# Optimization experiments

Measured on AMD Instinct MI355X. Metric: run time of the kernel, lower is better.

The kernel has to match this reference:

```python
import jax, jax.numpy as jnp
import numpy as np

B, T, D, H = 2, 2048, 1024, 16
DH = D // H


def setup_inputs() -> dict:
    key = jax.random.key(0)
    ks = jax.random.split(key, 5)
    s = 1.0 / np.sqrt(D)
    return {
        "x": jax.random.normal(ks[0], (B, T, D), dtype=jnp.float32),
        "Wq": jax.random.normal(ks[1], (D, D), dtype=jnp.float32) * s,
        "Wk": jax.random.normal(ks[2], (D, D), dtype=jnp.float32) * s,
        "Wv": jax.random.normal(ks[3], (D, D), dtype=jnp.float32) * s,
        "Wo": jax.random.normal(ks[4], (D, D), dtype=jnp.float32) * s,
    }


def reference(x, Wq, Wk, Wv, Wo):
    # torch nn.Linear(bias=False): y = x @ W.T, weight shape [out, in]
    q = (x @ Wq.T).reshape(B, T, H, DH).transpose(0, 2, 1, 3)  # [B,H,T,Dh]
    k = (x @ Wk.T).reshape(B, T, H, DH).transpose(0, 2, 1, 3)
    v = (x @ Wv.T).reshape(B, T, H, DH).transpose(0, 2, 1, 3)
    scores = jnp.einsum("bhqd,bhkd->bhqk", q, k) / jnp.sqrt(jnp.float32(DH))
    att = jax.nn.softmax(scores, axis=-1)
    y = jnp.einsum("bhqk,bhkd->bhqd", att, v)  # [B,H,T,Dh]
    y = y.transpose(0, 2, 1, 3).reshape(B, T, D)
    return y @ Wo.T
```

## Files before the change

kernel.cpp:

```cpp
#include <hip/hip_runtime.h>
#include <math.h>

typedef __attribute__((ext_vector_type(8))) _Float16 half8;
typedef __attribute__((ext_vector_type(4))) _Float16 half4;
typedef __attribute__((ext_vector_type(4))) float f32x4;

namespace {
constexpr int T_ = 2048, DH_ = 64;
constexpr int M_ = 4096;
constexpr int KD = 1024;
}

__global__ __launch_bounds__(256)
void conv_half4(const float* __restrict__ s0, const float* __restrict__ s1,
                const float* __restrict__ s2, const float* __restrict__ s3,
                _Float16* __restrict__ dst)
{
    const float* s = (blockIdx.y == 0) ? s0 : (blockIdx.y == 1) ? s1
                   : (blockIdx.y == 2) ? s2 : s3;
    const size_t i = ((size_t)blockIdx.x * 256 + threadIdx.x) * 8;
    const float4 a = *reinterpret_cast<const float4*>(s + i);
    const float4 b = *reinterpret_cast<const float4*>(s + i + 4);
    half8 h;
    h[0] = (_Float16)a.x; h[1] = (_Float16)a.y; h[2] = (_Float16)a.z; h[3] = (_Float16)a.w;
    h[4] = (_Float16)b.x; h[5] = (_Float16)b.y; h[6] = (_Float16)b.z; h[7] = (_Float16)b.w;
    *reinterpret_cast<half8*>(dst + (size_t)blockIdx.y * 1048576 + i) = h;
}

template <int BN>
__global__ __launch_bounds__(256)
void gemm_half(const _Float16* __restrict__ A, const _Float16* __restrict__ Bw,
               float* __restrict__ Cout,
               _Float16* __restrict__ qh, _Float16* __restrict__ kh,
               _Float16* __restrict__ vh, const int mode)
{
    constexpr int NF = BN / 32;
    __shared__ _Float16 As[128 * 64];
    __shared__ _Float16 Bs[BN * 64];
    const int tid = threadIdx.x;
    const int l   = tid & 63;
    const int w   = tid >> 6;
    const int wm  = w >> 1, wn = w & 1;
    const int m0  = blockIdx.y * 128;
    const int n0  = blockIdx.x * BN;

    f32x4 acc[4][NF];
#pragma unroll
    for (int i = 0; i < 4; ++i)
#pragma unroll
        for (int j = 0; j < NF; ++j) acc[i][j] = (f32x4){0.f, 0.f, 0.f, 0.f};

    const int srow = l >> 3;
    const int scol = ((l & 7) ^ srow) << 3;
    const int frow = l & 15;
    const int fkb  = (l >> 4) << 4;

    for (int kt = 0; kt < 16; ++kt) {
        const int kOff = kt << 6;
#pragma unroll
        for (int s = 0; s < 4; ++s) {
            const int j = (w << 2) + s;
            const _Float16* gp = A + (size_t)(m0 + (j << 3) + srow) * KD + kOff + scol;
            __builtin_amdgcn_global_load_lds(
                (const __attribute__((address_space(1))) void*)gp,
                (__attribute__((address_space(3))) void*)(As + (j << 9)), 16, 0, 0);
        }
#pragma unroll
        for (int s = 0; s < BN / 32; ++s) {
            const int j = w * (BN / 32) + s;
            const _Float16* gp = Bw + (size_t)(n0 + (j << 3) + srow) * KD + kOff + scol;
            __builtin_amdgcn_global_load_lds(
                (const __attribute__((address_space(1))) void*)gp,
                (__attribute__((address_space(3))) void*)(Bs + (j << 9)), 16, 0, 0);
        }
        __syncthreads();
#pragma unroll
        for (int ks = 0; ks < 2; ++ks) {
            half8 af[4], bfr[NF];
#pragma unroll
            for (int fi = 0; fi < 4; ++fi) {
                const int row = wm * 64 + fi * 16 + frow;
                const int cb  = (ks * 64 + fkb) ^ ((row & 7) << 4);
                af[fi] = *reinterpret_cast<const half8*>(
                    reinterpret_cast<const char*>(As) + row * 128 + cb);
            }
#pragma unroll
            for (int fj = 0; fj < NF; ++fj) {
                const int row = wn * (NF * 16) + fj * 16 + frow;
                const int cb  = (ks * 64 + fkb) ^ ((row & 7) << 4);
                bfr[fj] = *reinterpret_cast<const half8*>(
                    reinterpret_cast<const char*>(Bs) + row * 128 + cb);
            }
#pragma unroll
            for (int fi = 0; fi < 4; ++fi)
#pragma unroll
                for (int fj = 0; fj < NF; ++fj)
                    acc[fi][fj] = __builtin_amdgcn_mfma_f32_16x16x32_f16(
                        af[fi], bfr[fj], acc[fi][fj], 0, 0, 0);
        }
        __syncthreads();
    }

    const int r0 = (l >> 4) << 2;
    const float QSC = 0.125f * 1.44269504f;
#pragma unroll
    for (int fi = 0; fi < 4; ++fi)
#pragma unroll
        for (int fj = 0; fj < NF; ++fj)
#pragma unroll
            for (int r = 0; r < 4; ++r) {
                const int m = m0 + wm * 64 + fi * 16 + r0 + r;
                const int n = n0 + wn * (NF * 16) + fj * 16 + (l & 15);
                const float vv = acc[fi][fj][r];
                if (mode == 0) {
                    const int bb = m >> 11, t = m & 2047;
                    const int which = n >> 10, nl = n & 1023;
                    const int hh = nl >> 6, dh = nl & 63;
                    const int bh = (bb << 4) + hh;
                    if (which == 0)
                        qh[(((size_t)bh << 11) + t) * 64 + dh] = (_Float16)(vv * QSC);
                    else if (which == 1)
                        kh[(((size_t)bh << 11) + t) * 64 + dh] = (_Float16)vv;
                    else
                        vh[(((size_t)bh << 6) + dh) * 2048 + t] = (_Float16)vv;
                } else {
                    Cout[(size_t)m * 1024 + n] = vv;
                }
            }
}

#define SWZ(row, bytecol) (((row) << 7) + ((bytecol) ^ (((row) & 7) << 4)))

__global__ __launch_bounds__(256)
void attn_mfma(const _Float16* __restrict__ Qh, const _Float16* __restrict__ Kh,
               const _Float16* __restrict__ Vh, _Float16* __restrict__ Yh)
{
    __shared__ _Float16 Ks[2][64 * 64];
    __shared__ _Float16 Vs[2][64 * 64];
    __shared__ _Float16 Ps[64 * 64];
    const int tid = threadIdx.x;
    const int l   = tid & 63;
    const int w   = tid >> 6;
    const int g4  = l >> 4;
    const int c16 = l & 15;
    const int bh  = blockIdx.y;
    const int t0  = blockIdx.x * 64;
    const size_t qkbase = (size_t)bh * T_ * DH_;
    const size_t vbase  = (size_t)bh * DH_ * T_;

    const int srow = l >> 3;
    const int scol = ((l & 7) ^ srow) << 3;

    half8 qf[2];
#pragma unroll
    for (int ks = 0; ks < 2; ++ks)
        qf[ks] = *reinterpret_cast<const half8*>(
            Qh + qkbase + (size_t)(t0 + w * 16 + c16) * 64 + ks * 32 + g4 * 8);

    half8 ones;
#pragma unroll
    for (int j = 0; j < 8; ++j) ones[j] = (_Float16)1.f;

#pragma unroll
    for (int s = 0; s < 2; ++s) {
        const int j   = (w << 1) + s;
        const int row = (j << 3) + srow;
        const _Float16* gk = Kh + qkbase + (size_t)row * 64 + scol;
        __builtin_amdgcn_global_load_lds(
            (const __attribute__((address_space(1))) void*)gk,
            (__attribute__((address_space(3))) void*)(&Ks[0][0] + (j << 9)), 16, 0, 0);
        const _Float16* gv = Vh + vbase + (size_t)row * T_ + scol;
        __builtin_amdgcn_global_load_lds(
            (const __attribute__((address_space(1))) void*)gv,
            (__attribute__((address_space(3))) void*)(&Vs[0][0] + (j << 9)), 16, 0, 0);
    }
    __syncthreads();

    f32x4 o[4], ol;
#pragma unroll
    for (int i = 0; i < 4; ++i) o[i] = (f32x4){0.f, 0.f, 0.f, 0.f};
    ol = (f32x4){0.f, 0.f, 0.f, 0.f};

    for (int ktile = 0; ktile < T_ / 64; ++ktile) {
        const int cur = ktile & 1;
        if (ktile + 1 < T_ / 64) {
            const int nxt = cur ^ 1;
#pragma unroll
            for (int s = 0; s < 2; ++s) {
                const int j   = (w << 1) + s;
                const int row = (j << 3) + srow;
                const _Float16* gk = Kh + qkbase +
                    (size_t)((ktile + 1) * 64 + row) * 64 + scol;
                __builtin_amdgcn_global_load_lds(
                    (const __attribute__((address_space(1))) void*)gk,
                    (__attribute__((address_space(3))) void*)(&Ks[nxt][0] + (j << 9)), 16, 0, 0);
                const _Float16* gv = Vh + vbase + (size_t)row * T_ +
                    (ktile + 1) * 64 + scol;
                __builtin_amdgcn_global_load_lds(
                    (const __attribute__((address_space(1))) void*)gv,
                    (__attribute__((address_space(3))) void*)(&Vs[nxt][0] + (j << 9)), 16, 0, 0);
            }
        }

        const char* ksBase = reinterpret_cast<const char*>(&Ks[cur][0]);
        const char* vsBase = reinterpret_cast<const char*>(&Vs[cur][0]);
        f32x4 s[4];
#pragma unroll
        for (int fj = 0; fj < 4; ++fj) s[fj] = (f32x4){0.f, 0.f, 0.f, 0.f};
        __builtin_amdgcn_s_setprio(1);
#pragma unroll
        for (int ks = 0; ks < 2; ++ks)
#pragma unroll
            for (int fj = 0; fj < 4; ++fj) {
                const int row = fj * 16 + c16;
                const half8 kf = *reinterpret_cast<const half8*>(
                    ksBase + SWZ(row, ks * 64 + (g4 << 4)));
                s[fj] = __builtin_amdgcn_mfma_f32_16x16x32_f16(kf, qf[ks], s[fj], 0, 0, 0);
            }
        __builtin_amdgcn_s_setprio(0);

        {
            const int q = w * 16 + c16;
#pragma unroll
            for (int fj = 0; fj < 4; ++fj) {
                half4 p4;
#pragma unroll
                for (int r4 = 0; r4 < 4; ++r4)
                    p4[r4] = (_Float16)__builtin_amdgcn_exp2f(
                        fminf(s[fj][r4], 15.9f));
                *reinterpret_cast<half4*>(reinterpret_cast<char*>(Ps) +
                    SWZ(q, fj * 32 + (g4 << 3))) = p4;
            }
        }

        __builtin_amdgcn_s_setprio(1);
#pragma unroll
        for (int ks = 0; ks < 2; ++ks) {
            const int prow = w * 16 + c16;
            const half8 pf = *reinterpret_cast<const half8*>(
                reinterpret_cast<const char*>(Ps) + SWZ(prow, ks * 64 + (g4 << 4)));
#pragma unroll
            for (int fj = 0; fj < 4; ++fj) {
                const int vrow = fj * 16 + c16;
                const half8 vf = *reinterpret_cast<const half8*>(
                    vsBase + SWZ(vrow, ks * 64 + (g4 << 4)));
                o[fj] = __builtin_amdgcn_mfma_f32_16x16x32_f16(pf, vf, o[fj], 0, 0, 0);
            }
            ol = __builtin_amdgcn_mfma_f32_16x16x32_f16(pf, ones, ol, 0, 0, 0);
        }
        __builtin_amdgcn_s_setprio(0);

        __syncthreads();
    }

    const int bb = bh >> 4, hh = bh & 15;
#pragma unroll
    for (int r4 = 0; r4 < 4; ++r4) {
        const int t = t0 + w * 16 + (g4 << 2) + r4;
        const float inv = 1.f / ol[r4];
        const size_t mrow = ((size_t)bb * T_ + t) * 1024;
#pragma unroll
        for (int fj = 0; fj < 4; ++fj) {
            const int col = hh * 64 + fj * 16 + c16;
            Yh[mrow + col] = (_Float16)(o[fj][r4] * inv);
        }
    }
}

extern "C" void kernel_launch(void* const* d_in, const int* in_sizes, int n_in,
                              void* d_out, int out_size, void* d_ws, size_t ws_size,
                              hipStream_t stream)
{
    const float* x  = (const float*)d_in[0];
    const float* Wq = (const float*)d_in[1];
    const float* Wk = (const float*)d_in[2];
    const float* Wv = (const float*)d_in[3];
    const float* Wo = (const float*)d_in[4];

    unsigned char* ws = (unsigned char*)d_ws;
    _Float16* xh = (_Float16*)ws;
    _Float16* wh = (_Float16*)(ws + (size_t) 8388608);
    _Float16* qh = (_Float16*)(ws + (size_t)16777216);
    _Float16* kh = (_Float16*)(ws + (size_t)25165824);
    _Float16* vh = (_Float16*)(ws + (size_t)33554432);
    _Float16* yh = xh;

    conv_half4<<<dim3(2048, 1), 256, 0, stream>>>(x, nullptr, nullptr, nullptr, xh);
    conv_half4<<<dim3(512, 4), 256, 0, stream>>>(Wq, Wk, Wv, Wo, wh);

    dim3 blk(256);
    dim3 g1(24, 32);
    gemm_half<128><<<g1, blk, 0, stream>>>(xh, wh, nullptr, qh, kh, vh, 0);

    dim3 ga(T_ / 64, 32);
    attn_mfma<<<ga, blk, 0, stream>>>(qh, kh, vh, yh);

    dim3 g2(16, 32);
    gemm_half<64><<<g2, blk, 0, stream>>>(yh, wh + (size_t)3072 * KD, (float*)d_out,
                                          nullptr, nullptr, nullptr, 1);
}
```

Measured before the change: 152.3 us.

## Double-buffer LDS tiles in projection GEMM to overlap loads with MFMA

The GEMM now allocates two LDS buffers for the A and B tiles. It prefetches the next k-tile with global_load_lds while MFMAs run on the current tile, which is meant to hide global-to-LDS latency behind compute. The larger LDS footprint may reduce occupancy. Synchronisation now relies on the single __syncthreads at the end of each iteration, and global_load_lds completion may need an explicit vmcnt wait.

```diff
diff --git a/kernel.cpp b/kernel.cpp
--- a/kernel.cpp
+++ b/kernel.cpp
@@ -35,8 +35,10 @@
                _Float16* __restrict__ vh, const int mode)
 {
     constexpr int NF = BN / 32;
-    __shared__ _Float16 As[128 * 64];
-    __shared__ _Float16 Bs[BN * 64];
+    constexpr int ASZ = 128 * 64;
+    constexpr int BSZ = BN * 64;
+    __shared__ _Float16 As[2 * ASZ];
+    __shared__ _Float16 Bs[2 * BSZ];
     const int tid = threadIdx.x;
     const int l   = tid & 63;
     const int w   = tid >> 6;
@@ -55,25 +57,49 @@
     const int frow = l & 15;
     const int fkb  = (l >> 4) << 4;
 
+#pragma unroll
+    for (int s = 0; s < 4; ++s) {
+        const int j = (w << 2) + s;
+        const _Float16* gp = A + (size_t)(m0 + (j << 3) + srow) * KD + scol;
+        __builtin_amdgcn_global_load_lds(
+            (const __attribute__((address_space(1))) void*)gp,
+            (__attribute__((address_space(3))) void*)(As + (j << 9)), 16, 0, 0);
+    }
+#pragma unroll
+    for (int s = 0; s < BN / 32; ++s) {
+        const int j = w * (BN / 32) + s;
+        const _Float16* gp = Bw + (size_t)(n0 + (j << 3) + srow) * KD + scol;
+        __builtin_amdgcn_global_load_lds(
+            (const __attribute__((address_space(1))) void*)gp,
+            (__attribute__((address_space(3))) void*)(Bs + (j << 9)), 16, 0, 0);
+    }
+    __syncthreads();
+
     for (int kt = 0; kt < 16; ++kt) {
-        const int kOff = kt << 6;
-#pragma unroll
-        for (int s = 0; s < 4; ++s) {
-            const int j = (w << 2) + s;
-            const _Float16* gp = A + (size_t)(m0 + (j << 3) + srow) * KD + kOff + scol;
-            __builtin_amdgcn_global_load_lds(
-                (const __attribute__((address_space(1))) void*)gp,
-                (__attribute__((address_space(3))) void*)(As + (j << 9)), 16, 0, 0);
-        }
-#pragma unroll
-        for (int s = 0; s < BN / 32; ++s) {
-            const int j = w * (BN / 32) + s;
-            const _Float16* gp = Bw + (size_t)(n0 + (j << 3) + srow) * KD + kOff + scol;
-            __builtin_amdgcn_global_load_lds(
-                (const __attribute__((address_space(1))) void*)gp,
-                (__attribute__((address_space(3))) void*)(Bs + (j << 9)), 16, 0, 0);
-        }
-        __syncthreads();
+        const int cur = kt & 1;
+        if (kt + 1 < 16) {
+            const int nxt = cur ^ 1;
+            const int kOff = (kt + 1) << 6;
+#pragma unroll
+            for (int s = 0; s < 4; ++s) {
+                const int j = (w << 2) + s;
+                const _Float16* gp = A + (size_t)(m0 + (j << 3) + srow) * KD + kOff + scol;
+                __builtin_amdgcn_global_load_lds(
+                    (const __attribute__((address_space(1))) void*)gp,
+                    (__attribute__((address_space(3))) void*)(As + nxt * ASZ + (j << 9)), 16, 0, 0);
+            }
+#pragma unroll
+            for (int s = 0; s < BN / 32; ++s) {
+                const int j = w * (BN / 32) + s;
+                const _Float16* gp = Bw + (size_t)(n0 + (j << 3) + srow) * KD + kOff + scol;
+                __builtin_amdgcn_global_load_lds(
+                    (const __attribute__((address_space(1))) void*)gp,
+                    (__attribute__((address_space(3))) void*)(Bs + nxt * BSZ + (j << 9)), 16, 0, 0);
+            }
+        }
+
+        const char* aB = reinterpret_cast<const char*>(As + cur * ASZ);
+        const char* bB = reinterpret_cast<const char*>(Bs + cur * BSZ);
 #pragma unroll
         for (int ks = 0; ks < 2; ++ks) {
             half8 af[4], bfr[NF];
@@ -81,15 +107,13 @@
             for (int fi = 0; fi < 4; ++fi) {
                 const int row = wm * 64 + fi * 16 + frow;
                 const int cb  = (ks * 64 + fkb) ^ ((row & 7) << 4);
-                af[fi] = *reinterpret_cast<const half8*>(
-                    reinterpret_cast<const char*>(As) + row * 128 + cb);
+                af[fi] = *reinterpret_cast<const half8*>(aB + row * 128 + cb);
             }
 #pragma unroll
             for (int fj = 0; fj < NF; ++fj) {
                 const int row = wn * (NF * 16) + fj * 16 + frow;
                 const int cb  = (ks * 64 + fkb) ^ ((row & 7) << 4);
-                bfr[fj] = *reinterpret_cast<const half8*>(
-                    reinterpret_cast<const char*>(Bs) + row * 128 + cb);
+                bfr[fj] = *reinterpret_cast<const half8*>(bB + row * 128 + cb);
             }
 #pragma unroll
             for (int fi = 0; fi < 4; ++fi)
```

After: 155.7 us. 1.02x slower.

## Process 128 query rows per attention block to reuse K/V tiles

Applied to the files above, without the earlier changes.

Each attention block now handles 128 queries instead of 64, with every wave computing two 16-row query chunks that share the same K and V fragments loaded from LDS. This halves the global K/V traffic and the LDS fragment reads per query, and it doubles the MFMA work per barrier. In exchange the grid shrinks to 512 blocks, and register use and the P buffer in LDS both grow, which may reduce occupancy.

```diff
diff --git a/kernel.cpp b/kernel.cpp
--- a/kernel.cpp
+++ b/kernel.cpp
@@ -137,25 +137,28 @@
 {
     __shared__ _Float16 Ks[2][64 * 64];
     __shared__ _Float16 Vs[2][64 * 64];
-    __shared__ _Float16 Ps[64 * 64];
+    __shared__ _Float16 Ps[128 * 64];
     const int tid = threadIdx.x;
     const int l   = tid & 63;
     const int w   = tid >> 6;
     const int g4  = l >> 4;
     const int c16 = l & 15;
     const int bh  = blockIdx.y;
-    const int t0  = blockIdx.x * 64;
+    const int t0  = blockIdx.x * 128;
     const size_t qkbase = (size_t)bh * T_ * DH_;
     const size_t vbase  = (size_t)bh * DH_ * T_;
 
     const int srow = l >> 3;
     const int scol = ((l & 7) ^ srow) << 3;
 
-    half8 qf[2];
-#pragma unroll
-    for (int ks = 0; ks < 2; ++ks)
-        qf[ks] = *reinterpret_cast<const half8*>(
-            Qh + qkbase + (size_t)(t0 + w * 16 + c16) * 64 + ks * 32 + g4 * 8);
+    half8 qf[2][2];
+#pragma unroll
+    for (int c = 0; c < 2; ++c)
+#pragma unroll
+        for (int ks = 0; ks < 2; ++ks)
+            qf[c][ks] = *reinterpret_cast<const half8*>(
+                Qh + qkbase + (size_t)(t0 + 32 * w + 16 * c + c16) * 64
+                    + ks * 32 + g4 * 8);
 
     half8 ones;
 #pragma unroll
@@ -176,10 +179,13 @@
     }
     __syncthreads();
 
-    f32x4 o[4], ol;
-#pragma unroll
-    for (int i = 0; i < 4; ++i) o[i] = (f32x4){0.f, 0.f, 0.f, 0.f};
-    ol = (f32x4){0.f, 0.f, 0.f, 0.f};
+    f32x4 o[2][4], ol[2];
+#pragma unroll
+    for (int c = 0; c < 2; ++c) {
+#pragma unroll
+        for (int i = 0; i < 4; ++i) o[c][i] = (f32x4){0.f, 0.f, 0.f, 0.f};
+        ol[c] = (f32x4){0.f, 0.f, 0.f, 0.f};
+    }
 
     for (int ktile = 0; ktile < T_ / 64; ++ktile) {
         const int cur = ktile & 1;
@@ -204,9 +210,11 @@
 
         const char* ksBase = reinterpret_cast<const char*>(&Ks[cur][0]);
         const char* vsBase = reinterpret_cast<const char*>(&Vs[cur][0]);
-        f32x4 s[4];
-#pragma unroll
-        for (int fj = 0; fj < 4; ++fj) s[fj] = (f32x4){0.f, 0.f, 0.f, 0.f};
+        f32x4 s[2][4];
+#pragma unroll
+        for (int c = 0; c < 2; ++c)
+#pragma unroll
+            for (int fj = 0; fj < 4; ++fj) s[c][fj] = (f32x4){0.f, 0.f, 0.f, 0.f};
         __builtin_amdgcn_s_setprio(1);
 #pragma unroll
         for (int ks = 0; ks < 2; ++ks)
@@ -215,19 +223,21 @@
                 const int row = fj * 16 + c16;
                 const half8 kf = *reinterpret_cast<const half8*>(
                     ksBase + SWZ(row, ks * 64 + (g4 << 4)));
-                s[fj] = __builtin_amdgcn_mfma_f32_16x16x32_f16(kf, qf[ks], s[fj], 0, 0, 0);
+                s[0][fj] = __builtin_amdgcn_mfma_f32_16x16x32_f16(kf, qf[0][ks], s[0][fj], 0, 0, 0);
+                s[1][fj] = __builtin_amdgcn_mfma_f32_16x16x32_f16(kf, qf[1][ks], s[1][fj], 0, 0, 0);
             }
         __builtin_amdgcn_s_setprio(0);
 
-        {
-            const int q = w * 16 + c16;
+#pragma unroll
+        for (int c = 0; c < 2; ++c) {
+            const int q = 32 * w + 16 * c + c16;
 #pragma unroll
             for (int fj = 0; fj < 4; ++fj) {
                 half4 p4;
 #pragma unroll
                 for (int r4 = 0; r4 < 4; ++r4)
                     p4[r4] = (_Float16)__builtin_amdgcn_exp2f(
-                        fminf(s[fj][r4], 15.9f));
+                        fminf(s[c][fj][r4], 15.9f));
                 *reinterpret_cast<half4*>(reinterpret_cast<char*>(Ps) +
                     SWZ(q, fj * 32 + (g4 << 3))) = p4;
             }
@@ -236,17 +246,20 @@
         __builtin_amdgcn_s_setprio(1);
 #pragma unroll
         for (int ks = 0; ks < 2; ++ks) {
-            const int prow = w * 16 + c16;
-            const half8 pf = *reinterpret_cast<const half8*>(
-                reinterpret_cast<const char*>(Ps) + SWZ(prow, ks * 64 + (g4 << 4)));
+            const half8 pf0 = *reinterpret_cast<const half8*>(
+                reinterpret_cast<const char*>(Ps) + SWZ(32 * w + c16, ks * 64 + (g4 << 4)));
+            const half8 pf1 = *reinterpret_cast<const half8*>(
+                reinterpret_cast<const char*>(Ps) + SWZ(32 * w + 16 + c16, ks * 64 + (g4 << 4)));
 #pragma unroll
             for (int fj = 0; fj < 4; ++fj) {
                 const int vrow = fj * 16 + c16;
                 const half8 vf = *reinterpret_cast<const half8*>(
                     vsBase + SWZ(vrow, ks * 64 + (g4 << 4)));
-                o[fj] = __builtin_amdgcn_mfma_f32_16x16x32_f16(pf, vf, o[fj], 0, 0, 0);
-            }
-            ol = __builtin_amdgcn_mfma_f32_16x16x32_f16(pf, ones, ol, 0, 0, 0);
+                o[0][fj] = __builtin_amdgcn_mfma_f32_16x16x32_f16(pf0, vf, o[0][fj], 0, 0, 0);
+                o[1][fj] = __builtin_amdgcn_mfma_f32_16x16x32_f16(pf1, vf, o[1][fj], 0, 0, 0);
+            }
+            ol[0] = __builtin_amdgcn_mfma_f32_16x16x32_f16(pf0, ones, ol[0], 0, 0, 0);
+            ol[1] = __builtin_amdgcn_mfma_f32_16x16x32_f16(pf1, ones, ol[1], 0, 0, 0);
         }
         __builtin_amdgcn_s_setprio(0);
 
@@ -255,16 +268,18 @@
 
     const int bb = bh >> 4, hh = bh & 15;
 #pragma unroll
-    for (int r4 = 0; r4 < 4; ++r4) {
-        const int t = t0 + w * 16 + (g4 << 2) + r4;
-        const float inv = 1.f / ol[r4];
-        const size_t mrow = ((size_t)bb * T_ + t) * 1024;
-#pragma unroll
-        for (int fj = 0; fj < 4; ++fj) {
-            const int col = hh * 64 + fj * 16 + c16;
-            Yh[mrow + col] = (_Float16)(o[fj][r4] * inv);
-        }
-    }
+    for (int c = 0; c < 2; ++c)
+#pragma unroll
+        for (int r4 = 0; r4 < 4; ++r4) {
+            const int t = t0 + 32 * w + 16 * c + (g4 << 2) + r4;
+            const float inv = 1.f / ol[c][r4];
+            const size_t mrow = ((size_t)bb * T_ + t) * 1024;
+#pragma unroll
+            for (int fj = 0; fj < 4; ++fj) {
+                const int col = hh * 64 + fj * 16 + c16;
+                Yh[mrow + col] = (_Float16)(o[c][fj][r4] * inv);
+            }
+        }
 }
 
 extern "C" void kernel_launch(void* const* d_in, const int* in_sizes, int n_in,
@@ -292,7 +307,7 @@
     dim3 g1(24, 32);
     gemm_half<128><<<g1, blk, 0, stream>>>(xh, wh, nullptr, qh, kh, vh, 0);
 
-    dim3 ga(T_ / 64, 32);
+    dim3 ga(T_ / 128, 32);
     attn_mfma<<<ga, blk, 0, stream>>>(qh, kh, vh, yh);
 
     dim3 g2(16, 32);
```

New measurement: 145.2 us. 1.05x faster.
